# Kernel optimization log

Measured on AMD Instinct MI355X. Metric: run time of the kernel, lower is better.

## Reference

```python
import jax, jax.numpy as jnp
import numpy as np

B, N, FIN, H, D = 8, 2048, 64, 4, 32
ALPHA = 0.2  # LeakyReLU negative slope


def setup_inputs() -> dict:
    key = jax.random.key(0)
    k1, k2, k3, k4 = jax.random.split(key, 4)
    h = jax.random.normal(k1, (B, N, FIN), dtype=jnp.float32)
    adj = jax.random.randint(k2, (B, N, N), 0, 2).astype(jnp.int32)
    # ensure self-loops so every softmax row has at least one unmasked entry
    idx = jnp.arange(N)
    adj = adj.at[:, idx, idx].set(1)
    W = jax.random.normal(k3, (FIN, H * D), dtype=jnp.float32) * 0.1
    a = jax.random.normal(k4, (H, 2 * D), dtype=jnp.float32) * 0.1
    return {"h": h, "adj": adj, "W": W, "a": a}


def reference(h, adj, W, a):
    # h: (B,N,Fin), adj: (B,N,N) int, W: (Fin,H*D), a: (H,2D)
    Bn, Nn, _ = h.shape
    Hh, twoD = a.shape
    Dd = twoD // 2
    Wh = (h @ W).reshape(Bn, Nn, Hh, Dd).transpose(0, 2, 1, 3)  # (B,H,N,D)
    # e_ij = leakyrelu(Wh_i . a1 + Wh_j . a2) -- avoids O(N^2 * 2D) concat
    src = jnp.einsum('bhnd,hd->bhn', Wh, a[:, :Dd])  # (B,H,N)
    dst = jnp.einsum('bhnd,hd->bhn', Wh, a[:, Dd:])  # (B,H,N)
    e = jax.nn.leaky_relu(src[:, :, :, None] + dst[:, :, None, :], negative_slope=ALPHA)  # (B,H,N,N)
    e = jnp.where(adj[:, None, :, :] == 0, -jnp.inf, e)
    attn = jax.nn.softmax(e, axis=-1)  # (B,H,N,N)
    out = jnp.einsum('bhij,bhjd->bhid', attn, Wh)  # (B,H,N,D)
    return out.transpose(0, 2, 1, 3).reshape(Bn, Nn, Hh * Dd)
```

## Files before the change

### kernel.cpp

```cpp
#include <hip/hip_runtime.h>

typedef short short8 __attribute__((ext_vector_type(8)));
typedef _Float16 half8 __attribute__((ext_vector_type(8)));
typedef _Float16 half2v __attribute__((ext_vector_type(2)));
typedef float floatx4 __attribute__((ext_vector_type(4)));

extern "C" __device__ _Float16 __ocml_exp2_f16(_Float16);

#define B_   8
#define N_   2048
#define FIN_ 64
#define H_   4
#define D_   32
#define HD_  128
#define ALPHA_ 0.2f
#define LOG2E_ 1.4426950408889634f


__global__ __launch_bounds__(256) void gat_prep4(
    const float* __restrict__ h, const float* __restrict__ W, const float* __restrict__ a,
    unsigned short* __restrict__ WhF, float* __restrict__ src, unsigned short* __restrict__ dstb)
{
    __shared__ float Ws[FIN_][HD_];
    __shared__ float hsT[FIN_][36];
    int bx = blockIdx.x;
    int b = bx >> 6;
    int n0 = (bx & 63) * 32;
    int tid = threadIdx.x;

    #pragma unroll
    for (int it = 0; it < 8; ++it) {
        int idx = it * 256 + tid;
        int k = idx >> 5, c4 = (idx & 31) << 2;
        *(float4*)&Ws[k][c4] = *(const float4*)&W[k * HD_ + c4];
    }
    #pragma unroll
    for (int it = 0; it < 8; ++it) {
        int idx = it * 256 + tid;
        int r = idx >> 6, k = idx & 63;
        hsT[k][r] = h[((size_t)b * N_ + n0 + r) * FIN_ + k];
    }
    __syncthreads();

    int c = tid & 127;
    int rq = tid >> 7;
    int hh = c >> 5, d = c & 31;
    float acc[16];
    #pragma unroll
    for (int r = 0; r < 16; ++r) acc[r] = 0.f;
    for (int k = 0; k < FIN_; ++k) {
        float wv = Ws[k][c];
        float4 h0 = *(const float4*)&hsT[k][rq * 16];
        float4 h1 = *(const float4*)&hsT[k][rq * 16 + 4];
        float4 h2 = *(const float4*)&hsT[k][rq * 16 + 8];
        float4 h3 = *(const float4*)&hsT[k][rq * 16 + 12];
        acc[0]  += h0.x * wv; acc[1]  += h0.y * wv; acc[2]  += h0.z * wv; acc[3]  += h0.w * wv;
        acc[4]  += h1.x * wv; acc[5]  += h1.y * wv; acc[6]  += h1.z * wv; acc[7]  += h1.w * wv;
        acc[8]  += h2.x * wv; acc[9]  += h2.y * wv; acc[10] += h2.z * wv; acc[11] += h2.w * wv;
        acc[12] += h3.x * wv; acc[13] += h3.y * wv; acc[14] += h3.z * wv; acc[15] += h3.w * wv;
    }

    {
        int half = d >> 4, n = d & 15;
        int j0 = n0 + rq * 16;
        int it0 = j0 >> 5;
        int g0 = (j0 >> 3) & 3;
        #pragma unroll
        for (int rr = 0; rr < 2; ++rr) {
            __attribute__((aligned(16))) unsigned pk4[4];
            #pragma unroll
            for (int q = 0; q < 4; ++q)
                pk4[q] = __builtin_bit_cast(unsigned,
                    __builtin_amdgcn_cvt_pkrtz(acc[rr * 8 + 2 * q], acc[rr * 8 + 2 * q + 1]));
            size_t fi = ((((size_t)b * H_ + hh) * 64 + it0) * 2 + half) * 64
                        + (size_t)(g0 + rr) * 16 + n;
            *(uint4*)&WhF[fi * 8] = *(uint4*)pk4;
        }
    }

    float a1v = a[hh * 64 + d];
    float a2v = a[hh * 64 + 32 + d];
    #pragma unroll
    for (int r = 0; r < 16; ++r) {
        float s1 = acc[r] * a1v;
        float s2 = acc[r] * a2v;
        #pragma unroll
        for (int off = 16; off >= 1; off >>= 1) {
            s1 += __shfl_xor(s1, off, 32);
            s2 += __shfl_xor(s2, off, 32);
        }
        if (d == 0) {
            int n = n0 + rq * 16 + r;
            src[(b * H_ + hh) * N_ + n] = s1 * LOG2E_;
            _Float16 hv = (_Float16)(s2 * LOG2E_);
            dstb[(b * H_ + hh) * N_ + n] = __builtin_bit_cast(unsigned short, hv);
        }
    }
}

__global__ __launch_bounds__(256, 4) void gat_main12(
    const int* __restrict__ adj, const unsigned short* __restrict__ WhF,
    const float* __restrict__ src, const unsigned short* __restrict__ dstb,
    float* __restrict__ out)
{
    __shared__ unsigned short dsts[H_ * N_];
    __shared__ unsigned adjW[16][68];

    int bx = blockIdx.x;
    int b  = bx >> 7;
    int i0 = (bx & 127) * 16;
    int tid = threadIdx.x;
    int wv = tid >> 6, l = tid & 63;

    #pragma unroll
    for (int it = 0; it < 4; ++it) {
        int idx = it * 256 + tid;
        int hh = idx >> 8, off = (idx & 255) * 8;
        *(uint4*)&dsts[hh * N_ + off] =
            *(const uint4*)&dstb[(size_t)(b * H_ + hh) * N_ + off];
    }

    const int* adjBase = adj + ((size_t)(b * N_ + i0 + wv * 4)) * N_ + l;

    int vals[16];
    #pragma unroll
    for (int rr = 0; rr < 4; ++rr)
        #pragma unroll
        for (int cc = 0; cc < 4; ++cc)
            vals[rr * 4 + cc] = adjBase[rr * N_ + cc * 64];

    int h = wv, g = l >> 4, m = l & 15;
    int g8 = g << 3;
    _Float16 sv = (_Float16)src[(b * H_ + h) * N_ + i0 + m];
    half2v s2; s2[0] = sv; s2[1] = sv;
    const _Float16 alf = (_Float16)0.2f;
    const unsigned short* WhB =
        WhF + ((size_t)(b * H_ + h) * 64) * 1024 + l * 8;
    const unsigned short* dstH = &dsts[h * N_];

    short8 onesS;
    #pragma unroll
    for (int q = 0; q < 8; ++q) onesS[q] = (short)0x3C00;
    half8 ones = __builtin_bit_cast(half8, onesS);

    floatx4 acc0 = {0.f, 0.f, 0.f, 0.f};
    floatx4 acc1 = {0.f, 0.f, 0.f, 0.f};
    floatx4 acc2 = {0.f, 0.f, 0.f, 0.f};

    short8 bf0_c = *(const short8*)&WhB[0];
    short8 bf1_c = *(const short8*)&WhB[512];
    uint4 dv_c;

    for (int q = 0; q < 8; ++q) {
        #pragma unroll
        for (int rr = 0; rr < 4; ++rr)
            #pragma unroll
            for (int cc = 0; cc < 4; ++cc) {
                unsigned long long mk = __ballot(vals[rr * 4 + cc] != 0);
                if (l == 0) {
                    int c = q * 4 + cc;
                    adjW[wv * 4 + rr][2 * c]     = (unsigned)mk;
                    adjW[wv * 4 + rr][2 * c + 1] = (unsigned)(mk >> 32);
                }
            }
        __syncthreads();
        if (q == 0) dv_c = *(const uint4*)&dstH[g8];

        if (q < 7) {
            #pragma unroll
            for (int rr = 0; rr < 4; ++rr)
                #pragma unroll
                for (int cc = 0; cc < 4; ++cc)
                    vals[rr * 4 + cc] = adjBase[rr * N_ + (q + 1) * 256 + cc * 64];
        }

        for (int jj = 0; jj < 8; ++jj) {
            int it = q * 8 + jj;
            int fn = (it + 1) * 1024;
            short8 bf0_n = *(const short8*)&WhB[fn];
            short8 bf1_n = *(const short8*)&WhB[fn + 512];
            int j0n = ((it + 1) << 5) + g8;
            uint4  dv_n  = *(const uint4*)&dstH[(j0n < N_) ? j0n : g8];

            unsigned sh = adjW[m][it] >> g8;
            const unsigned* du = (const unsigned*)&dv_c;
            __attribute__((aligned(16))) unsigned pk[4];
            #pragma unroll
            for (int c2 = 0; c2 < 4; ++c2) {
                half2v d2 = __builtin_bit_cast(half2v, du[c2]);
                half2v e2 = s2 + d2;
                half2v t2 = e2 * alf;
                e2 = __builtin_elementwise_max(e2, t2);
                half2v x2;
                x2[0] = __ocml_exp2_f16(e2[0]);
                x2[1] = __ocml_exp2_f16(e2[1]);
                unsigned mk = ((((sh >> (2 * c2 + 1)) & 1u) << 16)
                               | ((sh >> (2 * c2)) & 1u)) * 0x3C00u;
                x2 = x2 * __builtin_bit_cast(half2v, mk);
                pk[c2] = __builtin_bit_cast(unsigned, x2);
            }
            half8 af = __builtin_bit_cast(half8, *(uint4*)pk);
            acc0 = __builtin_amdgcn_mfma_f32_16x16x32_f16(
                       af, __builtin_bit_cast(half8, bf0_c), acc0, 0, 0, 0);
            acc1 = __builtin_amdgcn_mfma_f32_16x16x32_f16(
                       af, __builtin_bit_cast(half8, bf1_c), acc1, 0, 0, 0);
            acc2 = __builtin_amdgcn_mfma_f32_16x16x32_f16(af, ones, acc2, 0, 0, 0);
            bf0_c = bf0_n; bf1_c = bf1_n; dv_c = dv_n;
        }
    }

    #pragma unroll
    for (int r = 0; r < 4; ++r) {
        float inv = 1.f / acc2[r];
        size_t o = ((size_t)b * N_ + i0 + g * 4 + r) * HD_ + h * 32 + m;
        out[o]      = acc0[r] * inv;
        out[o + 16] = acc1[r] * inv;
    }
}

extern "C" void kernel_launch(void* const* d_in, const int* in_sizes, int n_in,
                              void* d_out, int out_size, void* d_ws, size_t ws_size,
                              hipStream_t stream) {
    const float* h   = (const float*)d_in[0];
    const int*   adj = (const int*)d_in[1];
    const float* W   = (const float*)d_in[2];
    const float* a   = (const float*)d_in[3];
    float* out = (float*)d_out;

    unsigned short* WhF  = (unsigned short*)d_ws;
    float*          src  = (float*)((char*)d_ws + 4u * 1024 * 1024);
    unsigned short* dstb = (unsigned short*)((char*)d_ws + 4u * 1024 * 1024 + 256u * 1024);

    gat_prep4<<<B_ * (N_ / 32), 256, 0, stream>>>(h, W, a, WhF, src, dstb);
    gat_main12<<<B_ * (N_ / 16), 256, 0, stream>>>(adj, WhF, src, dstb, out);
}
```

Before: 224.5 us.

## Process 32 query rows per block to reuse Wh and dst loads

Doubles the row tile of the main attention kernel from 16 to 32 rows per block, so each wave computes two 16-row MFMA tiles that share the same Wh B-fragments and dst values. This halves the per-row global traffic for WhF and the shared-memory staging of dst, and halves the number of blocks. In exchange, register use rises (32 prefetched adjacency values, six accumulators), the launch bound drops to 2 blocks per CU, and there are fewer blocks for load balancing. The adjacency bitmask writes are also merged into single 64-bit stores.

```diff
diff --git a/kernel.cpp b/kernel.cpp
--- a/kernel.cpp
+++ b/kernel.cpp
@@ -98,17 +98,17 @@
     }
 }
 
-__global__ __launch_bounds__(256, 4) void gat_main12(
+__global__ __launch_bounds__(256, 2) void gat_main13(
     const int* __restrict__ adj, const unsigned short* __restrict__ WhF,
     const float* __restrict__ src, const unsigned short* __restrict__ dstb,
     float* __restrict__ out)
 {
     __shared__ unsigned short dsts[H_ * N_];
-    __shared__ unsigned adjW[16][68];
+    __shared__ unsigned adjW[32][70];
 
     int bx = blockIdx.x;
-    int b  = bx >> 7;
-    int i0 = (bx & 127) * 16;
+    int b  = bx >> 6;
+    int i0 = (bx & 63) * 32;
     int tid = threadIdx.x;
     int wv = tid >> 6, l = tid & 63;
 
@@ -120,19 +120,21 @@
             *(const uint4*)&dstb[(size_t)(b * H_ + hh) * N_ + off];
     }
 
-    const int* adjBase = adj + ((size_t)(b * N_ + i0 + wv * 4)) * N_ + l;
-
-    int vals[16];
-    #pragma unroll
-    for (int rr = 0; rr < 4; ++rr)
+    const int* adjBase = adj + ((size_t)(b * N_ + i0 + wv * 8)) * N_ + l;
+
+    int vals[32];
+    #pragma unroll
+    for (int rr = 0; rr < 8; ++rr)
         #pragma unroll
         for (int cc = 0; cc < 4; ++cc)
             vals[rr * 4 + cc] = adjBase[rr * N_ + cc * 64];
 
     int h = wv, g = l >> 4, m = l & 15;
     int g8 = g << 3;
-    _Float16 sv = (_Float16)src[(b * H_ + h) * N_ + i0 + m];
-    half2v s2; s2[0] = sv; s2[1] = sv;
+    _Float16 svA = (_Float16)src[(b * H_ + h) * N_ + i0 + m];
+    _Float16 svB = (_Float16)src[(b * H_ + h) * N_ + i0 + 16 + m];
+    half2v s2A; s2A[0] = svA; s2A[1] = svA;
+    half2v s2B; s2B[0] = svB; s2B[1] = svB;
     const _Float16 alf = (_Float16)0.2f;
     const unsigned short* WhB =
         WhF + ((size_t)(b * H_ + h) * 64) * 1024 + l * 8;
@@ -143,9 +145,12 @@
     for (int q = 0; q < 8; ++q) onesS[q] = (short)0x3C00;
     half8 ones = __builtin_bit_cast(half8, onesS);
 
-    floatx4 acc0 = {0.f, 0.f, 0.f, 0.f};
-    floatx4 acc1 = {0.f, 0.f, 0.f, 0.f};
-    floatx4 acc2 = {0.f, 0.f, 0.f, 0.f};
+    floatx4 acc0A = {0.f, 0.f, 0.f, 0.f};
+    floatx4 acc1A = {0.f, 0.f, 0.f, 0.f};
+    floatx4 acc2A = {0.f, 0.f, 0.f, 0.f};
+    floatx4 acc0B = {0.f, 0.f, 0.f, 0.f};
+    floatx4 acc1B = {0.f, 0.f, 0.f, 0.f};
+    floatx4 acc2B = {0.f, 0.f, 0.f, 0.f};
 
     short8 bf0_c = *(const short8*)&WhB[0];
     short8 bf1_c = *(const short8*)&WhB[512];
@@ -153,22 +158,19 @@
 
     for (int q = 0; q < 8; ++q) {
         #pragma unroll
-        for (int rr = 0; rr < 4; ++rr)
+        for (int rr = 0; rr < 8; ++rr)
             #pragma unroll
             for (int cc = 0; cc < 4; ++cc) {
                 unsigned long long mk = __ballot(vals[rr * 4 + cc] != 0);
-                if (l == 0) {
-                    int c = q * 4 + cc;
-                    adjW[wv * 4 + rr][2 * c]     = (unsigned)mk;
-                    adjW[wv * 4 + rr][2 * c + 1] = (unsigned)(mk >> 32);
-                }
+                if (l == 0)
+                    *(unsigned long long*)&adjW[wv * 8 + rr][2 * (q * 4 + cc)] = mk;
             }
         __syncthreads();
         if (q == 0) dv_c = *(const uint4*)&dstH[g8];
 
         if (q < 7) {
             #pragma unroll
-            for (int rr = 0; rr < 4; ++rr)
+            for (int rr = 0; rr < 8; ++rr)
                 #pragma unroll
                 for (int cc = 0; cc < 4; ++cc)
                     vals[rr * 4 + cc] = adjBase[rr * N_ + (q + 1) * 256 + cc * 64];
@@ -182,39 +184,70 @@
             int j0n = ((it + 1) << 5) + g8;
             uint4  dv_n  = *(const uint4*)&dstH[(j0n < N_) ? j0n : g8];
 
-            unsigned sh = adjW[m][it] >> g8;
+            unsigned shA = adjW[m][it] >> g8;
+            unsigned shB = adjW[m + 16][it] >> g8;
             const unsigned* du = (const unsigned*)&dv_c;
-            __attribute__((aligned(16))) unsigned pk[4];
-            #pragma unroll
-            for (int c2 = 0; c2 < 4; ++c2) {
-                half2v d2 = __builtin_bit_cast(half2v, du[c2]);
-                half2v e2 = s2 + d2;
-                half2v t2 = e2 * alf;
-                e2 = __builtin_elementwise_max(e2, t2);
-                half2v x2;
-                x2[0] = __ocml_exp2_f16(e2[0]);
-                x2[1] = __ocml_exp2_f16(e2[1]);
-                unsigned mk = ((((sh >> (2 * c2 + 1)) & 1u) << 16)
-                               | ((sh >> (2 * c2)) & 1u)) * 0x3C00u;
-                x2 = x2 * __builtin_bit_cast(half2v, mk);
-                pk[c2] = __builtin_bit_cast(unsigned, x2);
+
+            {
+                __attribute__((aligned(16))) unsigned pk[4];
+                #pragma unroll
+                for (int c2 = 0; c2 < 4; ++c2) {
+                    half2v d2 = __builtin_bit_cast(half2v, du[c2]);
+                    half2v e2 = s2A + d2;
+                    half2v t2 = e2 * alf;
+                    e2 = __builtin_elementwise_max(e2, t2);
+                    half2v x2;
+                    x2[0] = __ocml_exp2_f16(e2[0]);
+                    x2[1] = __ocml_exp2_f16(e2[1]);
+                    unsigned mk = ((((shA >> (2 * c2 + 1)) & 1u) << 16)
+                                   | ((shA >> (2 * c2)) & 1u)) * 0x3C00u;
+                    x2 = x2 * __builtin_bit_cast(half2v, mk);
+                    pk[c2] = __builtin_bit_cast(unsigned, x2);
+                }
+                half8 af = __builtin_bit_cast(half8, *(uint4*)pk);
+                acc0A = __builtin_amdgcn_mfma_f32_16x16x32_f16(
+                            af, __builtin_bit_cast(half8, bf0_c), acc0A, 0, 0, 0);
+                acc1A = __builtin_amdgcn_mfma_f32_16x16x32_f16(
+                            af, __builtin_bit_cast(half8, bf1_c), acc1A, 0, 0, 0);
+                acc2A = __builtin_amdgcn_mfma_f32_16x16x32_f16(af, ones, acc2A, 0, 0, 0);
             }
-            half8 af = __builtin_bit_cast(half8, *(uint4*)pk);
-            acc0 = __builtin_amdgcn_mfma_f32_16x16x32_f16(
-                       af, __builtin_bit_cast(half8, bf0_c), acc0, 0, 0, 0);
-            acc1 = __builtin_amdgcn_mfma_f32_16x16x32_f16(
-                       af, __builtin_bit_cast(half8, bf1_c), acc1, 0, 0, 0);
-            acc2 = __builtin_amdgcn_mfma_f32_16x16x32_f16(af, ones, acc2, 0, 0, 0);
+            {
+                __attribute__((aligned(16))) unsigned pk[4];
+                #pragma unroll
+                for (int c2 = 0; c2 < 4; ++c2) {
+                    half2v d2 = __builtin_bit_cast(half2v, du[c2]);
+                    half2v e2 = s2B + d2;
+                    half2v t2 = e2 * alf;
+                    e2 = __builtin_elementwise_max(e2, t2);
+                    half2v x2;
+                    x2[0] = __ocml_exp2_f16(e2[0]);
+                    x2[1] = __ocml_exp2_f16(e2[1]);
+                    unsigned mk = ((((shB >> (2 * c2 + 1)) & 1u) << 16)
+                                   | ((shB >> (2 * c2)) & 1u)) * 0x3C00u;
+                    x2 = x2 * __builtin_bit_cast(half2v, mk);
+                    pk[c2] = __builtin_bit_cast(unsigned, x2);
+                }
+                half8 af = __builtin_bit_cast(half8, *(uint4*)pk);
+                acc0B = __builtin_amdgcn_mfma_f32_16x16x32_f16(
+                            af, __builtin_bit_cast(half8, bf0_c), acc0B, 0, 0, 0);
+                acc1B = __builtin_amdgcn_mfma_f32_16x16x32_f16(
+                            af, __builtin_bit_cast(half8, bf1_c), acc1B, 0, 0, 0);
+                acc2B = __builtin_amdgcn_mfma_f32_16x16x32_f16(af, ones, acc2B, 0, 0, 0);
+            }
             bf0_c = bf0_n; bf1_c = bf1_n; dv_c = dv_n;
         }
     }
 
     #pragma unroll
     for (int r = 0; r < 4; ++r) {
-        float inv = 1.f / acc2[r];
-        size_t o = ((size_t)b * N_ + i0 + g * 4 + r) * HD_ + h * 32 + m;
-        out[o]      = acc0[r] * inv;
-        out[o + 16] = acc1[r] * inv;
+        float invA = 1.f / acc2A[r];
+        size_t oA = ((size_t)b * N_ + i0 + g * 4 + r) * HD_ + h * 32 + m;
+        out[oA]      = acc0A[r] * invA;
+        out[oA + 16] = acc1A[r] * invA;
+        float invB = 1.f / acc2B[r];
+        size_t oB = ((size_t)b * N_ + i0 + 16 + g * 4 + r) * HD_ + h * 32 + m;
+        out[oB]      = acc0B[r] * invB;
+        out[oB + 16] = acc1B[r] * invB;
     }
 }
 
@@ -232,5 +265,5 @@
     unsigned short* dstb = (unsigned short*)((char*)d_ws + 4u * 1024 * 1024 + 256u * 1024);
 
     gat_prep4<<<B_ * (N_ / 32), 256, 0, stream>>>(h, W, a, WhF, src, dstb);
-    gat_main12<<<B_ * (N_ / 16), 256, 0, stream>>>(adj, WhF, src, dstb, out);
+    gat_main13<<<B_ * (N_ / 32), 256, 0, stream>>>(adj, WhF, src, dstb, out);
 }
```

Result: slower. 235.5 us (+4.9%).

## Deepen prefetch to two iterations and vectorize adjacency mask reads

Applied to the files above, without the earlier changes.

Extends the software pipeline in the main attention kernel so that WhF fragments and dst values are prefetched two iterations ahead instead of one. The inner loop is fully unrolled, and the adjacency bitmask words for each 8-iteration chunk are loaded as two 16-byte LDS reads instead of one scalar read per iteration. Ballot results are stored as a single 64-bit write, and the adjW row is padded to 72. The aim is to hide global-load latency better and cut LDS instruction count, at the cost of more live registers, which may threaten the 4-blocks-per-SM occupancy target.

```diff
diff --git a/kernel.cpp b/kernel.cpp
--- a/kernel.cpp
+++ b/kernel.cpp
@@ -98,13 +98,13 @@
     }
 }
 
-__global__ __launch_bounds__(256, 4) void gat_main12(
+__global__ __launch_bounds__(256, 4) void gat_main14(
     const int* __restrict__ adj, const unsigned short* __restrict__ WhF,
     const float* __restrict__ src, const unsigned short* __restrict__ dstb,
     float* __restrict__ out)
 {
     __shared__ unsigned short dsts[H_ * N_];
-    __shared__ unsigned adjW[16][68];
+    __shared__ unsigned adjW[16][72];
 
     int bx = blockIdx.x;
     int b  = bx >> 7;
@@ -147,9 +147,11 @@
     floatx4 acc1 = {0.f, 0.f, 0.f, 0.f};
     floatx4 acc2 = {0.f, 0.f, 0.f, 0.f};
 
-    short8 bf0_c = *(const short8*)&WhB[0];
-    short8 bf1_c = *(const short8*)&WhB[512];
-    uint4 dv_c;
+    short8 bf0_a = *(const short8*)&WhB[0];
+    short8 bf1_a = *(const short8*)&WhB[512];
+    short8 bf0_b = *(const short8*)&WhB[1024];
+    short8 bf1_b = *(const short8*)&WhB[1536];
+    uint4 dv_a, dv_b;
 
     for (int q = 0; q < 8; ++q) {
         #pragma unroll
@@ -157,14 +159,17 @@
             #pragma unroll
             for (int cc = 0; cc < 4; ++cc) {
                 unsigned long long mk = __ballot(vals[rr * 4 + cc] != 0);
-                if (l == 0) {
-                    int c = q * 4 + cc;
-                    adjW[wv * 4 + rr][2 * c]     = (unsigned)mk;
-                    adjW[wv * 4 + rr][2 * c + 1] = (unsigned)(mk >> 32);
-                }
+                if (l == 0)
+                    *(unsigned long long*)&adjW[wv * 4 + rr][2 * (q * 4 + cc)] = mk;
             }
         __syncthreads();
-        if (q == 0) dv_c = *(const uint4*)&dstH[g8];
+
+        uint4 shv0 = *(const uint4*)&adjW[m][q * 8];
+        uint4 shv1 = *(const uint4*)&adjW[m][q * 8 + 4];
+        if (q == 0) {
+            dv_a = *(const uint4*)&dstH[g8];
+            dv_b = *(const uint4*)&dstH[32 + g8];
+        }
 
         if (q < 7) {
             #pragma unroll
@@ -174,16 +179,18 @@
                     vals[rr * 4 + cc] = adjBase[rr * N_ + (q + 1) * 256 + cc * 64];
         }
 
+        #pragma unroll
         for (int jj = 0; jj < 8; ++jj) {
             int it = q * 8 + jj;
-            int fn = (it + 1) * 1024;
+            int fn = (it + 2) * 1024;
             short8 bf0_n = *(const short8*)&WhB[fn];
             short8 bf1_n = *(const short8*)&WhB[fn + 512];
-            int j0n = ((it + 1) << 5) + g8;
-            uint4  dv_n  = *(const uint4*)&dstH[(j0n < N_) ? j0n : g8];
-
-            unsigned sh = adjW[m][it] >> g8;
-            const unsigned* du = (const unsigned*)&dv_c;
+            int j2 = ((it + 2) << 5) + g8;
+            uint4  dv_n = *(const uint4*)&dstH[(j2 < N_) ? j2 : g8];
+
+            unsigned sh = (jj < 4 ? ((const unsigned*)&shv0)[jj]
+                                  : ((const unsigned*)&shv1)[jj - 4]) >> g8;
+            const unsigned* du = (const unsigned*)&dv_a;
             __attribute__((aligned(16))) unsigned pk[4];
             #pragma unroll
             for (int c2 = 0; c2 < 4; ++c2) {
@@ -201,11 +208,13 @@
             }
             half8 af = __builtin_bit_cast(half8, *(uint4*)pk);
             acc0 = __builtin_amdgcn_mfma_f32_16x16x32_f16(
-                       af, __builtin_bit_cast(half8, bf0_c), acc0, 0, 0, 0);
+                       af, __builtin_bit_cast(half8, bf0_a), acc0, 0, 0, 0);
             acc1 = __builtin_amdgcn_mfma_f32_16x16x32_f16(
-                       af, __builtin_bit_cast(half8, bf1_c), acc1, 0, 0, 0);
+                       af, __builtin_bit_cast(half8, bf1_a), acc1, 0, 0, 0);
             acc2 = __builtin_amdgcn_mfma_f32_16x16x32_f16(af, ones, acc2, 0, 0, 0);
-            bf0_c = bf0_n; bf1_c = bf1_n; dv_c = dv_n;
+            bf0_a = bf0_b; bf0_b = bf0_n;
+            bf1_a = bf1_b; bf1_b = bf1_n;
+            dv_a = dv_b;   dv_b = dv_n;
         }
     }
 
@@ -232,5 +241,5 @@
     unsigned short* dstb = (unsigned short*)((char*)d_ws + 4u * 1024 * 1024 + 256u * 1024);
 
     gat_prep4<<<B_ * (N_ / 32), 256, 0, stream>>>(h, W, a, WhF, src, dstb);
-    gat_main12<<<B_ * (N_ / 16), 256, 0, stream>>>(adj, WhF, src, dstb, out);
+    gat_main14<<<B_ * (N_ / 16), 256, 0, stream>>>(adj, WhF, src, dstb, out);
 }
```

Result: faster. 218.9 us (-2.5%).

## Split key range across waves with all heads per wave and LDS reduction

Applied to the files above, without the earlier changes.

Each wave now handles one quarter of the key columns for all four heads, rather than one head across all columns. Adjacency is read directly per lane as int4 vectors and folded into the exponent as a large negative half-precision bias, which removes the ballot/LDS bitmask stage and the per-chunk block barriers. The wave-partial numerators and denominators are combined through a shared buffer at the end. In exchange it needs more accumulator registers (twelve floatx4) and several barriers in the epilogue. It also relies on the bias driving exp2 to zero in fp16, which changes how masking is done numerically.

```diff
diff --git a/kernel.cpp b/kernel.cpp
--- a/kernel.cpp
+++ b/kernel.cpp
@@ -98,123 +98,158 @@
     }
 }
 
-__global__ __launch_bounds__(256, 4) void gat_main12(
+__global__ __launch_bounds__(256, 4) void gat_main21(
     const int* __restrict__ adj, const unsigned short* __restrict__ WhF,
     const float* __restrict__ src, const unsigned short* __restrict__ dstb,
     float* __restrict__ out)
 {
-    __shared__ unsigned short dsts[H_ * N_];
-    __shared__ unsigned adjW[16][68];
+    __shared__ unsigned short dsts[H_][N_];
+    __shared__ float pbuf[4][4][64][4];
 
     int bx = blockIdx.x;
     int b  = bx >> 7;
     int i0 = (bx & 127) * 16;
     int tid = threadIdx.x;
     int wv = tid >> 6, l = tid & 63;
-
-    #pragma unroll
-    for (int it = 0; it < 4; ++it) {
-        int idx = it * 256 + tid;
-        int hh = idx >> 8, off = (idx & 255) * 8;
-        *(uint4*)&dsts[hh * N_ + off] =
-            *(const uint4*)&dstb[(size_t)(b * H_ + hh) * N_ + off];
-    }
-
-    const int* adjBase = adj + ((size_t)(b * N_ + i0 + wv * 4)) * N_ + l;
-
-    int vals[16];
-    #pragma unroll
-    for (int rr = 0; rr < 4; ++rr)
-        #pragma unroll
-        for (int cc = 0; cc < 4; ++cc)
-            vals[rr * 4 + cc] = adjBase[rr * N_ + cc * 64];
-
-    int h = wv, g = l >> 4, m = l & 15;
+    int g = l >> 4, m = l & 15;
     int g8 = g << 3;
-    _Float16 sv = (_Float16)src[(b * H_ + h) * N_ + i0 + m];
-    half2v s2; s2[0] = sv; s2[1] = sv;
+
+    {
+        int j0 = wv * 512;
+        #pragma unroll
+        for (int hh = 0; hh < 4; ++hh)
+            *(uint4*)&dsts[hh][j0 + l * 8] =
+                *(const uint4*)&dstb[(size_t)(b * H_ + hh) * N_ + j0 + l * 8];
+    }
+
+    half2v s2h[4];
+    #pragma unroll
+    for (int hh = 0; hh < 4; ++hh) {
+        _Float16 sv = (_Float16)src[(b * H_ + hh) * N_ + i0 + m];
+        s2h[hh][0] = sv; s2h[hh][1] = sv;
+    }
     const _Float16 alf = (_Float16)0.2f;
-    const unsigned short* WhB =
-        WhF + ((size_t)(b * H_ + h) * 64) * 1024 + l * 8;
-    const unsigned short* dstH = &dsts[h * N_];
+
+    const int* adjP = adj + ((size_t)(b * N_ + i0 + m)) * N_ + wv * 512 + g8;
+    const unsigned short* WhBw = WhF + (((size_t)b * H_) * 64 + wv * 16) * 1024 + l * 8;
+    const unsigned short* dvb = &dsts[0][wv * 512 + g8];
 
     short8 onesS;
     #pragma unroll
     for (int q = 0; q < 8; ++q) onesS[q] = (short)0x3C00;
     half8 ones = __builtin_bit_cast(half8, onesS);
 
-    floatx4 acc0 = {0.f, 0.f, 0.f, 0.f};
-    floatx4 acc1 = {0.f, 0.f, 0.f, 0.f};
-    floatx4 acc2 = {0.f, 0.f, 0.f, 0.f};
-
-    short8 bf0_c = *(const short8*)&WhB[0];
-    short8 bf1_c = *(const short8*)&WhB[512];
-    uint4 dv_c;
-
-    for (int q = 0; q < 8; ++q) {
-        #pragma unroll
-        for (int rr = 0; rr < 4; ++rr)
-            #pragma unroll
-            for (int cc = 0; cc < 4; ++cc) {
-                unsigned long long mk = __ballot(vals[rr * 4 + cc] != 0);
-                if (l == 0) {
-                    int c = q * 4 + cc;
-                    adjW[wv * 4 + rr][2 * c]     = (unsigned)mk;
-                    adjW[wv * 4 + rr][2 * c + 1] = (unsigned)(mk >> 32);
-                }
-            }
-        __syncthreads();
-        if (q == 0) dv_c = *(const uint4*)&dstH[g8];
-
-        if (q < 7) {
-            #pragma unroll
-            for (int rr = 0; rr < 4; ++rr)
-                #pragma unroll
-                for (int cc = 0; cc < 4; ++cc)
-                    vals[rr * 4 + cc] = adjBase[rr * N_ + (q + 1) * 256 + cc * 64];
-        }
-
-        for (int jj = 0; jj < 8; ++jj) {
-            int it = q * 8 + jj;
-            int fn = (it + 1) * 1024;
-            short8 bf0_n = *(const short8*)&WhB[fn];
-            short8 bf1_n = *(const short8*)&WhB[fn + 512];
-            int j0n = ((it + 1) << 5) + g8;
-            uint4  dv_n  = *(const uint4*)&dstH[(j0n < N_) ? j0n : g8];
-
-            unsigned sh = adjW[m][it] >> g8;
-            const unsigned* du = (const unsigned*)&dv_c;
+    floatx4 acc0[4], acc1[4], acc2[4];
+    #pragma unroll
+    for (int hh = 0; hh < 4; ++hh) {
+        acc0[hh] = floatx4{0.f, 0.f, 0.f, 0.f};
+        acc1[hh] = floatx4{0.f, 0.f, 0.f, 0.f};
+        acc2[hh] = floatx4{0.f, 0.f, 0.f, 0.f};
+    }
+
+    auto mkpair = [](int px, int py) -> unsigned {
+        unsigned t = (((unsigned)px) | ((unsigned)py << 16)) ^ 0x00010001u;
+        return t * 0xFC00u;
+    };
+
+    short8 bf0_1 = *(const short8*)&WhBw[0];
+    short8 bf1_1 = *(const short8*)&WhBw[512];
+    short8 bf0_2 = *(const short8*)&WhBw[65536];
+    short8 bf1_2 = *(const short8*)&WhBw[65536 + 512];
+    uint4 dv_1 = *(const uint4*)&dvb[0];
+    uint4 dv_2 = *(const uint4*)&dvb[2048];
+    int4 ajA0 = *(const int4*)&adjP[0];
+    int4 ajA1 = *(const int4*)&adjP[4];
+    int4 ajB0 = *(const int4*)&adjP[32];
+    int4 ajB1 = *(const int4*)&adjP[36];
+
+    for (int c = 0; c < 16; ++c) {
+        unsigned mk[4];
+        mk[0] = mkpair(ajA0.x, ajA0.y);
+        mk[1] = mkpair(ajA0.z, ajA0.w);
+        mk[2] = mkpair(ajA1.x, ajA1.y);
+        mk[3] = mkpair(ajA1.z, ajA1.w);
+        int cp = (c + 2 < 16) ? (c + 2) : 15;
+        int4 ajN0 = *(const int4*)&adjP[cp * 32];
+        int4 ajN1 = *(const int4*)&adjP[cp * 32 + 4];
+
+        #pragma unroll
+        for (int hh = 0; hh < 4; ++hh) {
+            int c2 = c + (hh >> 1);
+            int h2 = (hh + 2) & 3;
+            short8 bf0_n = *(const short8*)&WhBw[h2 * 65536 + c2 * 1024];
+            short8 bf1_n = *(const short8*)&WhBw[h2 * 65536 + c2 * 1024 + 512];
+            uint4  dv_n  = *(const uint4*)&dvb[h2 * 2048 + c2 * 32];
+
+            const unsigned* du = (const unsigned*)&dv_1;
             __attribute__((aligned(16))) unsigned pk[4];
             #pragma unroll
-            for (int c2 = 0; c2 < 4; ++c2) {
-                half2v d2 = __builtin_bit_cast(half2v, du[c2]);
-                half2v e2 = s2 + d2;
+            for (int p = 0; p < 4; ++p) {
+                half2v d2 = __builtin_bit_cast(half2v, du[p]);
+                half2v e2 = s2h[hh] + d2;
+                e2 = e2 + __builtin_bit_cast(half2v, mk[p]);
                 half2v t2 = e2 * alf;
                 e2 = __builtin_elementwise_max(e2, t2);
                 half2v x2;
                 x2[0] = __ocml_exp2_f16(e2[0]);
                 x2[1] = __ocml_exp2_f16(e2[1]);
-                unsigned mk = ((((sh >> (2 * c2 + 1)) & 1u) << 16)
-                               | ((sh >> (2 * c2)) & 1u)) * 0x3C00u;
-                x2 = x2 * __builtin_bit_cast(half2v, mk);
-                pk[c2] = __builtin_bit_cast(unsigned, x2);
+                pk[p] = __builtin_bit_cast(unsigned, x2);
             }
             half8 af = __builtin_bit_cast(half8, *(uint4*)pk);
-            acc0 = __builtin_amdgcn_mfma_f32_16x16x32_f16(
-                       af, __builtin_bit_cast(half8, bf0_c), acc0, 0, 0, 0);
-            acc1 = __builtin_amdgcn_mfma_f32_16x16x32_f16(
-                       af, __builtin_bit_cast(half8, bf1_c), acc1, 0, 0, 0);
-            acc2 = __builtin_amdgcn_mfma_f32_16x16x32_f16(af, ones, acc2, 0, 0, 0);
-            bf0_c = bf0_n; bf1_c = bf1_n; dv_c = dv_n;
-        }
-    }
-
+            acc0[hh] = __builtin_amdgcn_mfma_f32_16x16x32_f16(
+                           af, __builtin_bit_cast(half8, bf0_1), acc0[hh], 0, 0, 0);
+            acc1[hh] = __builtin_amdgcn_mfma_f32_16x16x32_f16(
+                           af, __builtin_bit_cast(half8, bf1_1), acc1[hh], 0, 0, 0);
+            acc2[hh] = __builtin_amdgcn_mfma_f32_16x16x32_f16(af, ones, acc2[hh], 0, 0, 0);
+            bf0_1 = bf0_2; bf0_2 = bf0_n;
+            bf1_1 = bf1_2; bf1_2 = bf1_n;
+            dv_1 = dv_2;   dv_2 = dv_n;
+        }
+        ajA0 = ajB0; ajA1 = ajB1;
+        ajB0 = ajN0; ajB1 = ajN1;
+    }
+
+    __syncthreads();
+    #pragma unroll
+    for (int hh = 0; hh < 4; ++hh)
+        *(floatx4*)&pbuf[wv][hh][l][0] = acc2[hh];
+    __syncthreads();
+    floatx4 sum2 = {0.f, 0.f, 0.f, 0.f};
+    #pragma unroll
+    for (int w2 = 0; w2 < 4; ++w2)
+        sum2 += *(const floatx4*)&pbuf[w2][wv][l][0];
+    floatx4 invv;
+    #pragma unroll
+    for (int r = 0; r < 4; ++r) invv[r] = 1.f / sum2[r];
+
+    __syncthreads();
+    #pragma unroll
+    for (int hh = 0; hh < 4; ++hh)
+        *(floatx4*)&pbuf[wv][hh][l][0] = acc0[hh];
+    __syncthreads();
+    floatx4 s0 = {0.f, 0.f, 0.f, 0.f};
+    #pragma unroll
+    for (int w2 = 0; w2 < 4; ++w2)
+        s0 += *(const floatx4*)&pbuf[w2][wv][l][0];
     #pragma unroll
     for (int r = 0; r < 4; ++r) {
-        float inv = 1.f / acc2[r];
-        size_t o = ((size_t)b * N_ + i0 + g * 4 + r) * HD_ + h * 32 + m;
-        out[o]      = acc0[r] * inv;
-        out[o + 16] = acc1[r] * inv;
+        size_t o = ((size_t)b * N_ + i0 + g * 4 + r) * HD_ + wv * 32 + m;
+        out[o] = s0[r] * invv[r];
+    }
+
+    __syncthreads();
+    #pragma unroll
+    for (int hh = 0; hh < 4; ++hh)
+        *(floatx4*)&pbuf[wv][hh][l][0] = acc1[hh];
+    __syncthreads();
+    floatx4 s1 = {0.f, 0.f, 0.f, 0.f};
+    #pragma unroll
+    for (int w2 = 0; w2 < 4; ++w2)
+        s1 += *(const floatx4*)&pbuf[w2][wv][l][0];
+    #pragma unroll
+    for (int r = 0; r < 4; ++r) {
+        size_t o = ((size_t)b * N_ + i0 + g * 4 + r) * HD_ + wv * 32 + m + 16;
+        out[o] = s1[r] * invv[r];
     }
 }
 
@@ -232,5 +267,5 @@
     unsigned short* dstb = (unsigned short*)((char*)d_ws + 4u * 1024 * 1024 + 256u * 1024);
 
     gat_prep4<<<B_ * (N_ / 32), 256, 0, stream>>>(h, W, a, WhF, src, dstb);
-    gat_main12<<<B_ * (N_ / 16), 256, 0, stream>>>(adj, WhF, src, dstb, out);
+    gat_main21<<<B_ * (N_ / 16), 256, 0, stream>>>(adj, WhF, src, dstb, out);
 }
```

New measurement: 241.3 us. 7.5% more time.
